# Optimization experiments

Hardware: AMD Instinct MI355X
Metric: run time of the kernel (lower is better)

Reference implementation:

```python
import jax, jax.numpy as jnp
import numpy as np

TEMPERATURE = 4.0

def setup_inputs() -> dict:
    key = jax.random.key(0)
    k1, k2 = jax.random.split(key)
    query = jax.random.normal(k1, (128, 128, 256), dtype=jnp.float32)      # (B, D, Q)
    context = jax.random.normal(k2, (128, 128, 32, 32), dtype=jnp.float32)  # (B, D, H, W)
    return {"query": query, "context": context}

def reference(query, context):
    B, D, Q = query.shape
    H, W = context.shape[2], context.shape[3]
    L = H * W  # context_length
    context_flat = context.reshape(B, D, L)                    # (B, D, L)
    # scores[b, l, q] = sum_d context[b, d, l] * query[b, d, q]
    scores = jnp.einsum('bdl,bdq->blq', context_flat, query)   # (B, L, Q)
    # first softmax: over query dim (context -> query)
    attn_q = jax.nn.softmax(scores, axis=-1)                   # (B, L, Q)
    # second softmax: over context dim with temperature (query -> context)
    attn_c = jax.nn.softmax(attn_q.transpose(0, 2, 1) * TEMPERATURE, axis=-1)  # (B, Q, L)
    # weighted_context[b, d, q] = sum_l context[b, d, l] * attn_c[b, q, l]
    weighted_context = jnp.einsum('bdl,bql->bdq', context_flat, attn_c)  # (B, D, Q)
    attention_map = attn_c.reshape(B, Q, H, W)
    return (weighted_context, attention_map)
```

## Files before the change

### kernel.cpp

```cpp
#include <hip/hip_runtime.h>
#include <math.h>

#define B_ 128
#define D_ 128
#define Q_ 256
#define L_ 1024

typedef __attribute__((ext_vector_type(8))) short s16x8;
typedef __attribute__((ext_vector_type(4))) float f32x4;
typedef unsigned short u16;

__device__ __forceinline__ u16 f2bf(float x) {
  unsigned u = __float_as_uint(x);
  u += 0x7FFF + ((u >> 16) & 1);
  return (u16)(u >> 16);
}
__device__ __forceinline__ float bf2f(u16 h) {
  return __uint_as_float(((unsigned)h) << 16);
}
__device__ __forceinline__ uint2 pack4bf(float4 v) {
  uint2 r;
  r.x = ((unsigned)f2bf(v.y) << 16) | (unsigned)f2bf(v.x);
  r.y = ((unsigned)f2bf(v.w) << 16) | (unsigned)f2bf(v.z);
  return r;
}
__device__ __forceinline__ void split8(const float* x, s16x8& hi, s16x8& lo) {
#pragma unroll
  for (int j = 0; j < 8; j++) {
    u16 h = f2bf(x[j]);
    hi[j] = (short)h;
    lo[j] = (short)f2bf(x[j] - bf2f(h));
  }
}

__global__ __launch_bounds__(256, 2) void k1_stats(
    const float* __restrict__ query, const float* __restrict__ ctx,
    float* __restrict__ pd, float* __restrict__ fmg, float* __restrict__ fsg) {
  __shared__ float sm[4][64], ss[4][64], fm[64], fs[64];
  const int lt = blockIdx.x, b = blockIdx.y;
  const int l0 = lt * 64;
  const int tid = threadIdx.x;
  const int wq = tid >> 6;
  const int lane = tid & 63, quad = lane >> 4, l15 = lane & 15;

  const float* Qb = query + (size_t)b * D_ * Q_;
  const float* Cb = ctx + (size_t)b * D_ * L_ + l0;

  f32x4 acc[4][4];
#pragma unroll
  for (int mi = 0; mi < 4; mi++)
#pragma unroll
    for (int ni = 0; ni < 4; ni++) acc[mi][ni] = (f32x4){0.f, 0.f, 0.f, 0.f};

#pragma unroll 2
  for (int k0 = 0; k0 < D_; k0 += 32) {
    const int kq = k0 + quad * 8;
    s16x8 ah[4], al[4], bh[4], bl[4];
#pragma unroll
    for (int mi = 0; mi < 4; mi++) {
      const float* p = Qb + (size_t)kq * Q_ + wq * 64 + mi * 16 + l15;
      float x[8];
#pragma unroll
      for (int j = 0; j < 8; j++) x[j] = p[(size_t)j * Q_];
      split8(x, ah[mi], al[mi]);
    }
#pragma unroll
    for (int ni = 0; ni < 4; ni++) {
      const float* p = Cb + (size_t)kq * L_ + ni * 16 + l15;
      float x[8];
#pragma unroll
      for (int j = 0; j < 8; j++) x[j] = p[(size_t)j * L_];
      split8(x, bh[ni], bl[ni]);
    }
#pragma unroll
    for (int mi = 0; mi < 4; mi++)
#pragma unroll
      for (int ni = 0; ni < 4; ni++) {
        acc[mi][ni] = __builtin_amdgcn_mfma_f32_16x16x32_bf16(
            ah[mi], bh[ni], acc[mi][ni], 0, 0, 0);
        acc[mi][ni] = __builtin_amdgcn_mfma_f32_16x16x32_bf16(
            ah[mi], bl[ni], acc[mi][ni], 0, 0, 0);
        acc[mi][ni] = __builtin_amdgcn_mfma_f32_16x16x32_bf16(
            al[mi], bh[ni], acc[mi][ni], 0, 0, 0);
      }
  }

#pragma unroll
  for (int ni = 0; ni < 4; ni++) {
    float m = -1e30f;
#pragma unroll
    for (int mi = 0; mi < 4; mi++)
#pragma unroll
      for (int r = 0; r < 4; r++) m = fmaxf(m, acc[mi][ni][r]);
    m = fmaxf(m, __shfl_xor(m, 16));
    m = fmaxf(m, __shfl_xor(m, 32));
    float s = 0.f;
#pragma unroll
    for (int mi = 0; mi < 4; mi++)
#pragma unroll
      for (int r = 0; r < 4; r++) s += __expf(acc[mi][ni][r] - m);
    s += __shfl_xor(s, 16);
    s += __shfl_xor(s, 32);
    if (quad == 0) {
      sm[wq][ni * 16 + l15] = m;
      ss[wq][ni * 16 + l15] = s;
    }
  }
  __syncthreads();
  if (tid < 64) {
    float m0 = sm[0][tid], m1 = sm[1][tid], m2 = sm[2][tid], m3 = sm[3][tid];
    float M = fmaxf(fmaxf(m0, m1), fmaxf(m2, m3));
    float S = ss[0][tid] * __expf(m0 - M) + ss[1][tid] * __expf(m1 - M) +
              ss[2][tid] * __expf(m2 - M) + ss[3][tid] * __expf(m3 - M);
    fm[tid] = M;
    fs[tid] = 1.f / S;
    fmg[(size_t)b * L_ + l0 + tid] = M;
    fsg[(size_t)b * L_ + l0 + tid] = 1.f / S;
  }
  __syncthreads();

  float fmv[4], fiv[4];
#pragma unroll
  for (int ni = 0; ni < 4; ni++) {
    fmv[ni] = fm[ni * 16 + l15];
    fiv[ni] = fs[ni * 16 + l15];
  }
  float dsum[4][4];
#pragma unroll
  for (int mi = 0; mi < 4; mi++)
#pragma unroll
    for (int r = 0; r < 4; r++) dsum[mi][r] = 0.f;
#pragma unroll
  for (int mi = 0; mi < 4; mi++)
#pragma unroll
    for (int r = 0; r < 4; r++) {
#pragma unroll
      for (int ni = 0; ni < 4; ni++) {
        float a = __expf(acc[mi][ni][r] - fmv[ni]) * fiv[ni];
        dsum[mi][r] += __expf(4.f * a);
      }
    }
#pragma unroll
  for (int mi = 0; mi < 4; mi++)
#pragma unroll
    for (int r = 0; r < 4; r++) {
      float v = dsum[mi][r];
      v += __shfl_xor(v, 1);
      v += __shfl_xor(v, 2);
      v += __shfl_xor(v, 4);
      v += __shfl_xor(v, 8);
      dsum[mi][r] = v;
    }
  if (l15 == 0) {
#pragma unroll
    for (int mi = 0; mi < 4; mi++)
#pragma unroll
      for (int r = 0; r < 4; r++)
        pd[(size_t)lt * (B_ * Q_) + b * Q_ + wq * 64 + mi * 16 + quad * 4 +
           r] = dsum[mi][r];
  }
}

__global__ __launch_bounds__(256, 2) void k3_fused(
    const float* __restrict__ query, const float* __restrict__ ctx,
    const float* __restrict__ pd, const float* __restrict__ fmg,
    const float* __restrict__ fsg, float* __restrict__ attn,
    float* __restrict__ W) {
  __shared__ u16 QsH[64][136], QsL[64][136];
  __shared__ u16 As[128][72];
  __shared__ u16 Bs[64][72];
  __shared__ float ivs[64];
  const int b = blockIdx.y, q0 = blockIdx.x * 64;
  const int tid = threadIdx.x;
  const int w = tid >> 6, lane = tid & 63, quad = lane >> 4, l15 = lane & 15;

  if (tid < 64) {
    float s = 0.f;
#pragma unroll
    for (int t = 0; t < 16; t++)
      s += pd[(size_t)t * (B_ * Q_) + b * Q_ + q0 + tid];
    ivs[tid] = 1.f / s;
  }
  {
    const int dr = tid >> 1;
    const int qc = (tid & 1) * 32;
    const float* qp = query + ((size_t)b * D_ + dr) * Q_ + q0 + qc;
#pragma unroll
    for (int c = 0; c < 8; c++) {
      float4 v = *(const float4*)(qp + c * 4);
      float xs[4] = {v.x, v.y, v.z, v.w};
#pragma unroll
      for (int j = 0; j < 4; j++) {
        u16 h = f2bf(xs[j]);
        QsH[qc + c * 4 + j][dr] = h;
        QsL[qc + c * 4 + j][dr] = f2bf(xs[j] - bf2f(h));
      }
    }
  }
  __syncthreads();

  float ivq[4];
#pragma unroll
  for (int ni = 0; ni < 4; ni++) ivq[ni] = ivs[ni * 16 + l15];
  const int wd = (w >> 1) * 64, wn = (w & 1) * 32;
  f32x4 accw[4][2];
#pragma unroll
  for (int mi = 0; mi < 4; mi++)
#pragma unroll
    for (int ni = 0; ni < 2; ni++) accw[mi][ni] = (f32x4){0.f, 0.f, 0.f, 0.f};

  const float* Cb = ctx + (size_t)b * D_ * L_;
  float* Mapb = attn + ((size_t)b * Q_ + q0) * L_;
  const float* fmb = fmg + (size_t)b * L_;
  const float* fsb = fsg + (size_t)b * L_;
  const int dd = tid >> 3;
  const int lc8 = (tid & 7) * 8;

  for (int l0 = 0; l0 < L_; l0 += 64) {
    if (l0) __syncthreads();
#pragma unroll
    for (int h = 0; h < 4; h++) {
      const int d = dd + h * 32;
      const float* cp = Cb + (size_t)d * L_ + l0 + lc8;
      float4 v0 = *(const float4*)cp;
      float4 v1 = *(const float4*)(cp + 4);
      *(uint2*)&As[d][lc8] = pack4bf(v0);
      *(uint2*)&As[d][lc8 + 4] = pack4bf(v1);
    }

    f32x4 accs[4];
#pragma unroll
    for (int ni = 0; ni < 4; ni++) accs[ni] = (f32x4){0.f, 0.f, 0.f, 0.f};
#pragma unroll
    for (int ks = 0; ks < 4; ks++) {
      const float* ap =
          Cb + (size_t)(ks * 32 + quad * 8) * L_ + l0 + 16 * w + l15;
      float x[8];
#pragma unroll
      for (int j = 0; j < 8; j++) x[j] = ap[(size_t)j * L_];
      s16x8 ch, cl;
      split8(x, ch, cl);
#pragma unroll
      for (int ni = 0; ni < 4; ni++) {
        const s16x8 qh = *(const s16x8*)&QsH[ni * 16 + l15][ks * 32 + quad * 8];
        const s16x8 ql = *(const s16x8*)&QsL[ni * 16 + l15][ks * 32 + quad * 8];
        accs[ni] =
            __builtin_amdgcn_mfma_f32_16x16x32_bf16(ch, qh, accs[ni], 0, 0, 0);
        accs[ni] =
            __builtin_amdgcn_mfma_f32_16x16x32_bf16(ch, ql, accs[ni], 0, 0, 0);
        accs[ni] =
            __builtin_amdgcn_mfma_f32_16x16x32_bf16(cl, qh, accs[ni], 0, 0, 0);
      }
    }

    float fml[4], fsl[4];
#pragma unroll
    for (int r = 0; r < 4; r++) {
      fml[r] = fmb[l0 + 16 * w + quad * 4 + r];
      fsl[r] = fsb[l0 + 16 * w + quad * 4 + r];
    }
#pragma unroll
    for (int ni = 0; ni < 4; ni++)
#pragma unroll
      for (int r = 0; r < 4; r++) {
        float a = __expf(accs[ni][r] - fml[r]) * fsl[r];
        float t = __expf(4.f * a) * ivq[ni];
        Mapb[(size_t)(ni * 16 + l15) * L_ + l0 + 16 * w + quad * 4 + r] = t;
        Bs[ni * 16 + l15][16 * w + quad * 4 + r] = f2bf(t);
      }
    __syncthreads();

#pragma unroll
    for (int ks2 = 0; ks2 < 2; ks2++) {
      s16x8 af[4], bq[2];
#pragma unroll
      for (int mi = 0; mi < 4; mi++)
        af[mi] = *(const s16x8*)&As[wd + mi * 16 + l15][ks2 * 32 + quad * 8];
#pragma unroll
      for (int ni = 0; ni < 2; ni++)
        bq[ni] = *(const s16x8*)&Bs[wn + ni * 16 + l15][ks2 * 32 + quad * 8];
#pragma unroll
      for (int mi = 0; mi < 4; mi++)
#pragma unroll
        for (int ni = 0; ni < 2; ni++)
          accw[mi][ni] = __builtin_amdgcn_mfma_f32_16x16x32_bf16(
              af[mi], bq[ni], accw[mi][ni], 0, 0, 0);
    }
  }

  float* Wb = W + (size_t)b * D_ * Q_;
#pragma unroll
  for (int mi = 0; mi < 4; mi++)
#pragma unroll
    for (int ni = 0; ni < 2; ni++)
#pragma unroll
      for (int r = 0; r < 4; r++)
        Wb[(size_t)(wd + mi * 16 + quad * 4 + r) * Q_ + q0 + wn + ni * 16 +
           l15] = accw[mi][ni][r];
}

__global__ __launch_bounds__(256, 2) void k1_attnq_legacy(
    const float* __restrict__ query, const float* __restrict__ ctx,
    float* __restrict__ attq, float* __restrict__ pd) {
  __shared__ float sm[4][64], ss[4][64], fm[64], fs[64];
  const int lt = blockIdx.x, b = blockIdx.y;
  const int l0 = lt * 64;
  const int tid = threadIdx.x;
  const int wq = tid >> 6;
  const int lane = tid & 63, quad = lane >> 4, l15 = lane & 15;

  const float* Qb = query + (size_t)b * D_ * Q_;
  const float* Cb = ctx + (size_t)b * D_ * L_ + l0;

  f32x4 acc[4][4];
#pragma unroll
  for (int mi = 0; mi < 4; mi++)
#pragma unroll
    for (int ni = 0; ni < 4; ni++) acc[mi][ni] = (f32x4){0.f, 0.f, 0.f, 0.f};

#pragma unroll 2
  for (int k0 = 0; k0 < D_; k0 += 32) {
    const int kq = k0 + quad * 8;
    s16x8 ah[4], al[4], bh[4], bl[4];
#pragma unroll
    for (int mi = 0; mi < 4; mi++) {
      const float* p = Qb + (size_t)kq * Q_ + wq * 64 + mi * 16 + l15;
      float x[8];
#pragma unroll
      for (int j = 0; j < 8; j++) x[j] = p[(size_t)j * Q_];
      split8(x, ah[mi], al[mi]);
    }
#pragma unroll
    for (int ni = 0; ni < 4; ni++) {
      const float* p = Cb + (size_t)kq * L_ + ni * 16 + l15;
      float x[8];
#pragma unroll
      for (int j = 0; j < 8; j++) x[j] = p[(size_t)j * L_];
      split8(x, bh[ni], bl[ni]);
    }
#pragma unroll
    for (int mi = 0; mi < 4; mi++)
#pragma unroll
      for (int ni = 0; ni < 4; ni++) {
        acc[mi][ni] = __builtin_amdgcn_mfma_f32_16x16x32_bf16(
            ah[mi], bh[ni], acc[mi][ni], 0, 0, 0);
        acc[mi][ni] = __builtin_amdgcn_mfma_f32_16x16x32_bf16(
            ah[mi], bl[ni], acc[mi][ni], 0, 0, 0);
        acc[mi][ni] = __builtin_amdgcn_mfma_f32_16x16x32_bf16(
            al[mi], bh[ni], acc[mi][ni], 0, 0, 0);
      }
  }

#pragma unroll
  for (int ni = 0; ni < 4; ni++) {
    float m = -1e30f;
#pragma unroll
    for (int mi = 0; mi < 4; mi++)
#pragma unroll
      for (int r = 0; r < 4; r++) m = fmaxf(m, acc[mi][ni][r]);
    m = fmaxf(m, __shfl_xor(m, 16));
    m = fmaxf(m, __shfl_xor(m, 32));
    float s = 0.f;
#pragma unroll
    for (int mi = 0; mi < 4; mi++)
#pragma unroll
      for (int r = 0; r < 4; r++) s += __expf(acc[mi][ni][r] - m);
    s += __shfl_xor(s, 16);
    s += __shfl_xor(s, 32);
    if (quad == 0) {
      sm[wq][ni * 16 + l15] = m;
      ss[wq][ni * 16 + l15] = s;
    }
  }
  __syncthreads();
  if (tid < 64) {
    float m0 = sm[0][tid], m1 = sm[1][tid], m2 = sm[2][tid], m3 = sm[3][tid];
    float M = fmaxf(fmaxf(m0, m1), fmaxf(m2, m3));
    float S = ss[0][tid] * __expf(m0 - M) + ss[1][tid] * __expf(m1 - M) +
              ss[2][tid] * __expf(m2 - M) + ss[3][tid] * __expf(m3 - M);
    fm[tid] = M;
    fs[tid] = 1.f / S;
  }
  __syncthreads();

  float fmv[4], fiv[4];
#pragma unroll
  for (int ni = 0; ni < 4; ni++) {
    fmv[ni] = fm[ni * 16 + l15];
    fiv[ni] = fs[ni * 16 + l15];
  }
  float* Ab = attq + ((size_t)b * Q_ + wq * 64) * L_ + l0;
  float dsum[4][4];
#pragma unroll
  for (int mi = 0; mi < 4; mi++)
#pragma unroll
    for (int r = 0; r < 4; r++) dsum[mi][r] = 0.f;
#pragma unroll
  for (int mi = 0; mi < 4; mi++)
#pragma unroll
    for (int r = 0; r < 4; r++) {
      const int q = mi * 16 + quad * 4 + r;
#pragma unroll
      for (int ni = 0; ni < 4; ni++) {
        float a = __expf(acc[mi][ni][r] - fmv[ni]) * fiv[ni];
        Ab[(size_t)q * L_ + ni * 16 + l15] = a;
        dsum[mi][r] += __expf(4.f * a);
      }
    }
#pragma unroll
  for (int mi = 0; mi < 4; mi++)
#pragma unroll
    for (int r = 0; r < 4; r++) {
      float v = dsum[mi][r];
      v += __shfl_xor(v, 1);
      v += __shfl_xor(v, 2);
      v += __shfl_xor(v, 4);
      v += __shfl_xor(v, 8);
      dsum[mi][r] = v;
    }
  if (l15 == 0) {
#pragma unroll
    for (int mi = 0; mi < 4; mi++)
#pragma unroll
      for (int r = 0; r < 4; r++)
        pd[(size_t)lt * (B_ * Q_) + b * Q_ + wq * 64 + mi * 16 + quad * 4 +
           r] = dsum[mi][r];
  }
}

__global__ __launch_bounds__(256) void k2_invd(const float* __restrict__ pd,
                                               float* __restrict__ invd) {
  const int i = blockIdx.x * 256 + threadIdx.x;
  float s = 0.f;
#pragma unroll
  for (int t = 0; t < 16; t++) s += pd[(size_t)t * (B_ * Q_) + i];
  invd[i] = 1.f / s;
}

__global__ __launch_bounds__(256) void k4_weighted(
    const float* __restrict__ ctx, float* __restrict__ attn,
    const float* __restrict__ invd, float* __restrict__ W) {
  __shared__ unsigned short As[128][32];
  __shared__ unsigned short Bs[64][32];
  const int b = blockIdx.y, q0 = blockIdx.x * 64;
  const int tid = threadIdx.x;
  const int w = tid >> 6, lane = tid & 63, quad = lane >> 4, l15 = lane & 15;
  const int wd = (w >> 1) * 64, wn = (w & 1) * 32;

  const float* Cb = ctx + (size_t)b * D_ * L_;
  float* Ab = attn + ((size_t)b * Q_ + q0) * L_;

  const int lc = (tid & 7) * 4;
  const int rr = tid >> 3;
  const float id0 = invd[b * Q_ + q0 + rr];
  const float id1 = invd[b * Q_ + q0 + rr + 32];

  f32x4 acc[4][2];
#pragma unroll
  for (int mi = 0; mi < 4; mi++)
#pragma unroll
    for (int ni = 0; ni < 2; ni++) acc[mi][ni] = (f32x4){0.f, 0.f, 0.f, 0.f};

  for (int l0 = 0; l0 < L_; l0 += 32) {
    if (l0) __syncthreads();
#pragma unroll
    for (int h = 0; h < 4; h++) {
      const int d = rr + h * 32;
      float4 cv = *(const float4*)(Cb + (size_t)d * L_ + l0 + lc);
      *(uint2*)&As[d][lc] = pack4bf(cv);
    }
#pragma unroll
    for (int h = 0; h < 2; h++) {
      const int q = rr + h * 32;
      float* p = Ab + (size_t)q * L_ + l0 + lc;
      float4 a = *(const float4*)p;
      const float idv = h ? id1 : id0;
      float4 t;
      t.x = __expf(4.f * a.x) * idv;
      t.y = __expf(4.f * a.y) * idv;
      t.z = __expf(4.f * a.z) * idv;
      t.w = __expf(4.f * a.w) * idv;
      *(float4*)p = t;
      *(uint2*)&Bs[q][lc] = pack4bf(t);
    }
    __syncthreads();

    s16x8 af[4], bq[2];
#pragma unroll
    for (int mi = 0; mi < 4; mi++)
      af[mi] = *(const s16x8*)&As[wd + mi * 16 + l15][quad * 8];
#pragma unroll
    for (int ni = 0; ni < 2; ni++)
      bq[ni] = *(const s16x8*)&Bs[wn + ni * 16 + l15][quad * 8];
#pragma unroll
    for (int mi = 0; mi < 4; mi++)
#pragma unroll
      for (int ni = 0; ni < 2; ni++)
        acc[mi][ni] = __builtin_amdgcn_mfma_f32_16x16x32_bf16(
            af[mi], bq[ni], acc[mi][ni], 0, 0, 0);
  }

  float* Wb = W + (size_t)b * D_ * Q_;
#pragma unroll
  for (int mi = 0; mi < 4; mi++)
#pragma unroll
    for (int ni = 0; ni < 2; ni++)
#pragma unroll
      for (int r = 0; r < 4; r++)
        Wb[(size_t)(wd + mi * 16 + quad * 4 + r) * Q_ + q0 + wn + ni * 16 +
           l15] = acc[mi][ni][r];
}

extern "C" void kernel_launch(void* const* d_in, const int* in_sizes, int n_in,
                              void* d_out, int out_size, void* d_ws,
                              size_t ws_size, hipStream_t stream) {
  (void)in_sizes;
  (void)n_in;
  (void)out_size;
  const float* query = (const float*)d_in[0];
  const float* ctx = (const float*)d_in[1];
  float* W = (float*)d_out;
  float* attn = (float*)d_out + (size_t)B_ * D_ * Q_;

  const size_t need =
      ((size_t)16 * B_ * Q_ + (size_t)2 * B_ * L_) * sizeof(float);
  if (d_ws && ws_size >= need) {
    float* pd = (float*)d_ws;
    float* fm = pd + (size_t)16 * B_ * Q_;
    float* fs = fm + (size_t)B_ * L_;
    k1_stats<<<dim3(L_ / 64, B_), 256, 0, stream>>>(query, ctx, pd, fm, fs);
    k3_fused<<<dim3(Q_ / 64, B_), 256, 0, stream>>>(query, ctx, pd, fm, fs,
                                                    attn, W);
  } else {
    const size_t need_pd = (size_t)17 * B_ * Q_ * sizeof(float);
    float* pd = (d_ws && ws_size >= need_pd) ? (float*)d_ws : W;
    float* invd = pd + (size_t)16 * B_ * Q_;
    k1_attnq_legacy<<<dim3(L_ / 64, B_), 256, 0, stream>>>(query, ctx, attn,
                                                           pd);
    k2_invd<<<dim3(B_ * Q_ / 256), 256, 0, stream>>>(pd, invd);
    k4_weighted<<<dim3(Q_ / 64, B_), 256, 0, stream>>>(ctx, attn, invd, W);
  }
}
```

Baseline: 300.3 us.

## Shrink per-block work tiles and raise occupancy in stats and fused kernels

k1_stats now runs 512 threads per block with 8 waves, each covering 32 query columns instead of 64. This halves accumulator registers, and the B split is interleaved with the MFMA loop to cut live registers further. k3_fused now tiles 32 query columns per block instead of 64, which doubles the grid and shrinks shared memory so more blocks fit per CU. The cost is that the context tile is reloaded and the QK score recomputed twice as often across q-blocks, which adds global traffic and redundant MFMA work.

```diff
diff --git a/kernel.cpp b/kernel.cpp
--- a/kernel.cpp
+++ b/kernel.cpp
@@ -33,10 +33,10 @@
   }
 }
 
-__global__ __launch_bounds__(256, 2) void k1_stats(
+__global__ __launch_bounds__(512, 4) void k1_stats(
     const float* __restrict__ query, const float* __restrict__ ctx,
     float* __restrict__ pd, float* __restrict__ fmg, float* __restrict__ fsg) {
-  __shared__ float sm[4][64], ss[4][64], fm[64], fs[64];
+  __shared__ float sm[8][64], ss[8][64], fm[64], fs[64];
   const int lt = blockIdx.x, b = blockIdx.y;
   const int l0 = lt * 64;
   const int tid = threadIdx.x;
@@ -46,19 +46,19 @@
   const float* Qb = query + (size_t)b * D_ * Q_;
   const float* Cb = ctx + (size_t)b * D_ * L_ + l0;
 
-  f32x4 acc[4][4];
-#pragma unroll
-  for (int mi = 0; mi < 4; mi++)
+  f32x4 acc[2][4];
+#pragma unroll
+  for (int mi = 0; mi < 2; mi++)
 #pragma unroll
     for (int ni = 0; ni < 4; ni++) acc[mi][ni] = (f32x4){0.f, 0.f, 0.f, 0.f};
 
 #pragma unroll 2
   for (int k0 = 0; k0 < D_; k0 += 32) {
     const int kq = k0 + quad * 8;
-    s16x8 ah[4], al[4], bh[4], bl[4];
-#pragma unroll
-    for (int mi = 0; mi < 4; mi++) {
-      const float* p = Qb + (size_t)kq * Q_ + wq * 64 + mi * 16 + l15;
+    s16x8 ah[2], al[2];
+#pragma unroll
+    for (int mi = 0; mi < 2; mi++) {
+      const float* p = Qb + (size_t)kq * Q_ + wq * 32 + mi * 16 + l15;
       float x[8];
 #pragma unroll
       for (int j = 0; j < 8; j++) x[j] = p[(size_t)j * Q_];
@@ -70,33 +70,32 @@
       float x[8];
 #pragma unroll
       for (int j = 0; j < 8; j++) x[j] = p[(size_t)j * L_];
-      split8(x, bh[ni], bl[ni]);
-    }
-#pragma unroll
-    for (int mi = 0; mi < 4; mi++)
-#pragma unroll
-      for (int ni = 0; ni < 4; ni++) {
-        acc[mi][ni] = __builtin_amdgcn_mfma_f32_16x16x32_bf16(
-            ah[mi], bh[ni], acc[mi][ni], 0, 0, 0);
-        acc[mi][ni] = __builtin_amdgcn_mfma_f32_16x16x32_bf16(
-            ah[mi], bl[ni], acc[mi][ni], 0, 0, 0);
-        acc[mi][ni] = __builtin_amdgcn_mfma_f32_16x16x32_bf16(
-            al[mi], bh[ni], acc[mi][ni], 0, 0, 0);
-      }
+      s16x8 bh, bl;
+      split8(x, bh, bl);
+#pragma unroll
+      for (int mi = 0; mi < 2; mi++) {
+        acc[mi][ni] = __builtin_amdgcn_mfma_f32_16x16x32_bf16(
+            ah[mi], bh, acc[mi][ni], 0, 0, 0);
+        acc[mi][ni] = __builtin_amdgcn_mfma_f32_16x16x32_bf16(
+            ah[mi], bl, acc[mi][ni], 0, 0, 0);
+        acc[mi][ni] = __builtin_amdgcn_mfma_f32_16x16x32_bf16(
+            al[mi], bh, acc[mi][ni], 0, 0, 0);
+      }
+    }
   }
 
 #pragma unroll
   for (int ni = 0; ni < 4; ni++) {
     float m = -1e30f;
 #pragma unroll
-    for (int mi = 0; mi < 4; mi++)
+    for (int mi = 0; mi < 2; mi++)
 #pragma unroll
       for (int r = 0; r < 4; r++) m = fmaxf(m, acc[mi][ni][r]);
     m = fmaxf(m, __shfl_xor(m, 16));
     m = fmaxf(m, __shfl_xor(m, 32));
     float s = 0.f;
 #pragma unroll
-    for (int mi = 0; mi < 4; mi++)
+    for (int mi = 0; mi < 2; mi++)
 #pragma unroll
       for (int r = 0; r < 4; r++) s += __expf(acc[mi][ni][r] - m);
     s += __shfl_xor(s, 16);
@@ -108,14 +107,17 @@
   }
   __syncthreads();
   if (tid < 64) {
-    float m0 = sm[0][tid], m1 = sm[1][tid], m2 = sm[2][tid], m3 = sm[3][tid];
-    float M = fmaxf(fmaxf(m0, m1), fmaxf(m2, m3));
-    float S = ss[0][tid] * __expf(m0 - M) + ss[1][tid] * __expf(m1 - M) +
-              ss[2][tid] * __expf(m2 - M) + ss[3][tid] * __expf(m3 - M);
+    float M = -1e30f;
+#pragma unroll
+    for (int t = 0; t < 8; t++) M = fmaxf(M, sm[t][tid]);
+    float S = 0.f;
+#pragma unroll
+    for (int t = 0; t < 8; t++) S += ss[t][tid] * __expf(sm[t][tid] - M);
+    const float iS = 1.f / S;
     fm[tid] = M;
-    fs[tid] = 1.f / S;
+    fs[tid] = iS;
     fmg[(size_t)b * L_ + l0 + tid] = M;
-    fsg[(size_t)b * L_ + l0 + tid] = 1.f / S;
+    fsg[(size_t)b * L_ + l0 + tid] = iS;
   }
   __syncthreads();
 
@@ -125,13 +127,13 @@
     fmv[ni] = fm[ni * 16 + l15];
     fiv[ni] = fs[ni * 16 + l15];
   }
-  float dsum[4][4];
-#pragma unroll
-  for (int mi = 0; mi < 4; mi++)
+  float dsum[2][4];
+#pragma unroll
+  for (int mi = 0; mi < 2; mi++)
 #pragma unroll
     for (int r = 0; r < 4; r++) dsum[mi][r] = 0.f;
 #pragma unroll
-  for (int mi = 0; mi < 4; mi++)
+  for (int mi = 0; mi < 2; mi++)
 #pragma unroll
     for (int r = 0; r < 4; r++) {
 #pragma unroll
@@ -141,7 +143,7 @@
       }
     }
 #pragma unroll
-  for (int mi = 0; mi < 4; mi++)
+  for (int mi = 0; mi < 2; mi++)
 #pragma unroll
     for (int r = 0; r < 4; r++) {
       float v = dsum[mi][r];
@@ -153,28 +155,28 @@
     }
   if (l15 == 0) {
 #pragma unroll
-    for (int mi = 0; mi < 4; mi++)
+    for (int mi = 0; mi < 2; mi++)
 #pragma unroll
       for (int r = 0; r < 4; r++)
-        pd[(size_t)lt * (B_ * Q_) + b * Q_ + wq * 64 + mi * 16 + quad * 4 +
+        pd[(size_t)lt * (B_ * Q_) + b * Q_ + wq * 32 + mi * 16 + quad * 4 +
            r] = dsum[mi][r];
   }
 }
 
-__global__ __launch_bounds__(256, 2) void k3_fused(
+__global__ __launch_bounds__(256, 4) void k3_fused(
     const float* __restrict__ query, const float* __restrict__ ctx,
     const float* __restrict__ pd, const float* __restrict__ fmg,
     const float* __restrict__ fsg, float* __restrict__ attn,
     float* __restrict__ W) {
-  __shared__ u16 QsH[64][136], QsL[64][136];
-  __shared__ u16 As[128][72];
-  __shared__ u16 Bs[64][72];
-  __shared__ float ivs[64];
-  const int b = blockIdx.y, q0 = blockIdx.x * 64;
+  __shared__ u16 QsH[32][132], QsL[32][132];
+  __shared__ u16 As[128][68];
+  __shared__ u16 Bs[32][68];
+  __shared__ float ivs[32];
+  const int b = blockIdx.y, q0 = blockIdx.x * 32;
   const int tid = threadIdx.x;
   const int w = tid >> 6, lane = tid & 63, quad = lane >> 4, l15 = lane & 15;
 
-  if (tid < 64) {
+  if (tid < 32) {
     float s = 0.f;
 #pragma unroll
     for (int t = 0; t < 16; t++)
@@ -183,10 +185,10 @@
   }
   {
     const int dr = tid >> 1;
-    const int qc = (tid & 1) * 32;
+    const int qc = (tid & 1) * 16;
     const float* qp = query + ((size_t)b * D_ + dr) * Q_ + q0 + qc;
 #pragma unroll
-    for (int c = 0; c < 8; c++) {
+    for (int c = 0; c < 4; c++) {
       float4 v = *(const float4*)(qp + c * 4);
       float xs[4] = {v.x, v.y, v.z, v.w};
 #pragma unroll
@@ -199,13 +201,13 @@
   }
   __syncthreads();
 
-  float ivq[4];
-#pragma unroll
-  for (int ni = 0; ni < 4; ni++) ivq[ni] = ivs[ni * 16 + l15];
-  const int wd = (w >> 1) * 64, wn = (w & 1) * 32;
-  f32x4 accw[4][2];
-#pragma unroll
-  for (int mi = 0; mi < 4; mi++)
+  float ivq[2];
+#pragma unroll
+  for (int ni = 0; ni < 2; ni++) ivq[ni] = ivs[ni * 16 + l15];
+  const int wd = w * 32;
+  f32x4 accw[2][2];
+#pragma unroll
+  for (int mi = 0; mi < 2; mi++)
 #pragma unroll
     for (int ni = 0; ni < 2; ni++) accw[mi][ni] = (f32x4){0.f, 0.f, 0.f, 0.f};
 
@@ -228,9 +230,9 @@
       *(uint2*)&As[d][lc8 + 4] = pack4bf(v1);
     }
 
-    f32x4 accs[4];
-#pragma unroll
-    for (int ni = 0; ni < 4; ni++) accs[ni] = (f32x4){0.f, 0.f, 0.f, 0.f};
+    f32x4 accs[2];
+#pragma unroll
+    for (int ni = 0; ni < 2; ni++) accs[ni] = (f32x4){0.f, 0.f, 0.f, 0.f};
 #pragma unroll
     for (int ks = 0; ks < 4; ks++) {
       const float* ap =
@@ -241,7 +243,7 @@
       s16x8 ch, cl;
       split8(x, ch, cl);
 #pragma unroll
-      for (int ni = 0; ni < 4; ni++) {
+      for (int ni = 0; ni < 2; ni++) {
         const s16x8 qh = *(const s16x8*)&QsH[ni * 16 + l15][ks * 32 + quad * 8];
         const s16x8 ql = *(const s16x8*)&QsL[ni * 16 + l15][ks * 32 + quad * 8];
         accs[ni] =
@@ -260,7 +262,7 @@
       fsl[r] = fsb[l0 + 16 * w + quad * 4 + r];
     }
 #pragma unroll
-    for (int ni = 0; ni < 4; ni++)
+    for (int ni = 0; ni < 2; ni++)
 #pragma unroll
       for (int r = 0; r < 4; r++) {
         float a = __expf(accs[ni][r] - fml[r]) * fsl[r];
@@ -272,15 +274,15 @@
 
 #pragma unroll
     for (int ks2 = 0; ks2 < 2; ks2++) {
-      s16x8 af[4], bq[2];
-#pragma unroll
-      for (int mi = 0; mi < 4; mi++)
+      s16x8 af[2], bq[2];
+#pragma unroll
+      for (int mi = 0; mi < 2; mi++)
         af[mi] = *(const s16x8*)&As[wd + mi * 16 + l15][ks2 * 32 + quad * 8];
 #pragma unroll
       for (int ni = 0; ni < 2; ni++)
-        bq[ni] = *(const s16x8*)&Bs[wn + ni * 16 + l15][ks2 * 32 + quad * 8];
-#pragma unroll
-      for (int mi = 0; mi < 4; mi++)
+        bq[ni] = *(const s16x8*)&Bs[ni * 16 + l15][ks2 * 32 + quad * 8];
+#pragma unroll
+      for (int mi = 0; mi < 2; mi++)
 #pragma unroll
         for (int ni = 0; ni < 2; ni++)
           accw[mi][ni] = __builtin_amdgcn_mfma_f32_16x16x32_bf16(
@@ -290,13 +292,13 @@
 
   float* Wb = W + (size_t)b * D_ * Q_;
 #pragma unroll
-  for (int mi = 0; mi < 4; mi++)
+  for (int mi = 0; mi < 2; mi++)
 #pragma unroll
     for (int ni = 0; ni < 2; ni++)
 #pragma unroll
       for (int r = 0; r < 4; r++)
-        Wb[(size_t)(wd + mi * 16 + quad * 4 + r) * Q_ + q0 + wn + ni * 16 +
-           l15] = accw[mi][ni][r];
+        Wb[(size_t)(wd + mi * 16 + quad * 4 + r) * Q_ + q0 + ni * 16 + l15] =
+            accw[mi][ni][r];
 }
 
 __global__ __launch_bounds__(256, 2) void k1_attnq_legacy(
@@ -528,8 +530,8 @@
     float* pd = (float*)d_ws;
     float* fm = pd + (size_t)16 * B_ * Q_;
     float* fs = fm + (size_t)B_ * L_;
-    k1_stats<<<dim3(L_ / 64, B_), 256, 0, stream>>>(query, ctx, pd, fm, fs);
-    k3_fused<<<dim3(Q_ / 64, B_), 256, 0, stream>>>(query, ctx, pd, fm, fs,
+    k1_stats<<<dim3(L_ / 64, B_), 512, 0, stream>>>(query, ctx, pd, fm, fs);
+    k3_fused<<<dim3(Q_ / 32, B_), 256, 0, stream>>>(query, ctx, pd, fm, fs,
                                                     attn, W);
   } else {
     const size_t need_pd = (size_t)17 * B_ * Q_ * sizeof(float);
```

Measured after the change: 388.1 us. +29.2%, slower.
